# Performance work log

Measured on AMD Instinct MI355X. Metric: run time of the kernel, lower is better.

Reference implementation:

```python
import jax, jax.numpy as jnp
import numpy as np

B, T, F = 1024, 512, 64
P, H = 64, 128  # proj_dim, hidden_size


def _init(key, shape, scale):
    return jax.random.normal(key, shape, dtype=jnp.float32) * scale


def setup_inputs() -> dict:
    key = jax.random.key(0)
    ks = jax.random.split(key, 20)
    sp = 1.0 / np.sqrt(P)
    sh = 1.0 / np.sqrt(H)
    return {
        "x": jax.random.normal(ks[0], (B, T, F), dtype=jnp.float32),
        "lengths": jax.random.randint(ks[1], (B,), 1, T, dtype=jnp.int64),
        # input projection
        "W_proj": _init(ks[2], (P, F), 1.0 / np.sqrt(F)),
        "b_proj": jnp.zeros((P,), jnp.float32),
        # LSTM layer 0 (input P -> hidden H), pytorch gate order i,f,g,o
        "W_ih0": _init(ks[3], (4 * H, P), sh),
        "W_hh0": _init(ks[4], (4 * H, H), sh),
        "b_ih0": _init(ks[5], (4 * H,), sh),
        "b_hh0": _init(ks[6], (4 * H,), sh),
        # LSTM layer 1 (input H -> hidden H)
        "W_ih1": _init(ks[7], (4 * H, H), sh),
        "W_hh1": _init(ks[8], (4 * H, H), sh),
        "b_ih1": _init(ks[9], (4 * H,), sh),
        "b_hh1": _init(ks[10], (4 * H,), sh),
        # MLP head: H -> H//2 -> 1 (dropout is identity in eval)
        "W_h1": _init(ks[11], (H // 2, H), sh),
        "b_h1": jnp.zeros((H // 2,), jnp.float32),
        "W_h2": _init(ks[12], (1, H // 2), 1.0 / np.sqrt(H // 2)),
        "b_h2": jnp.zeros((1,), jnp.float32),
    }


def lstm_layer(x_seq, W_ih, W_hh, b_ih, b_hh):
    # x_seq: [B, T, D]; precompute input contribution for all timesteps
    Hh = W_hh.shape[1]
    xg = jnp.einsum("btd,gd->btg", x_seq, W_ih) + b_ih + b_hh  # [B, T, 4H]
    xg_t = jnp.transpose(xg, (1, 0, 2))  # [T, B, 4H]
    Bn = x_seq.shape[0]
    h0 = jnp.zeros((Bn, Hh), x_seq.dtype)
    c0 = jnp.zeros((Bn, Hh), x_seq.dtype)

    def step(carry, g_in):
        h, c = carry
        g = g_in + h @ W_hh.T
        i, f, gg, o = jnp.split(g, 4, axis=-1)
        i = jax.nn.sigmoid(i)
        f = jax.nn.sigmoid(f)
        gg = jnp.tanh(gg)
        o = jax.nn.sigmoid(o)
        c = f * c + i * gg
        h = o * jnp.tanh(c)
        return (h, c), h

    _, hs = jax.lax.scan(step, (h0, c0), xg_t)  # hs: [T, B, H]
    return jnp.transpose(hs, (1, 0, 2))  # [B, T, H]


def reference(x, lengths, W_proj, b_proj, W_ih0, W_hh0, b_ih0, b_hh0,
              W_ih1, W_hh1, b_ih1, b_hh1, W_h1, b_h1, W_h2, b_h2):
    # eval mode: dropout layers are identity
    proj = jnp.einsum("btf,pf->btp", x, W_proj) + b_proj  # [B, T, P]
    h1 = lstm_layer(proj, W_ih0, W_hh0, b_ih0, b_hh0)
    h2 = lstm_layer(h1, W_ih1, W_hh1, b_ih1, b_hh1)
    last = h2[:, -1, :]  # [B, H]
    hid = jax.nn.relu(last @ W_h1.T + b_h1)
    logits = (hid @ W_h2.T + b_h2).squeeze(-1)  # [B]
    return logits
```

## Files before the change

### kernel.cpp

```cpp
#include <hip/hip_runtime.h>
#include <hip/hip_bf16.h>
#include <stdint.h>

typedef __bf16 bf16x8 __attribute__((ext_vector_type(8)));
typedef float  f32x4  __attribute__((ext_vector_type(4)));

#define BAR()  asm volatile("s_waitcnt lgkmcnt(0)\n\ts_barrier" ::: "memory")

static __device__ __forceinline__ float sigm(float x) {
  return __builtin_amdgcn_rcpf(1.0f + __builtin_amdgcn_exp2f(x * -1.4426950408889634f));
}
static __device__ __forceinline__ float tanh_fast(float x) {
  return 1.0f - 2.0f * __builtin_amdgcn_rcpf(1.0f + __builtin_amdgcn_exp2f(x * 2.8853900817779268f));
}
static __device__ __forceinline__ unsigned short f2bf(float f) {
  return __builtin_bit_cast(unsigned short, (__bf16)f);
}
static __device__ __forceinline__ float bf2f(unsigned short u) {
  union { uint32_t i; float f; } v; v.i = ((uint32_t)u) << 16; return v.f;
}
static __device__ __forceinline__ void async16(const float* g, float* l) {
  __builtin_amdgcn_global_load_lds((__attribute__((address_space(1))) void*)g,
                                   (__attribute__((address_space(3))) void*)l, 16, 0, 0);
}

__global__ __launch_bounds__(512) __attribute__((amdgpu_waves_per_eu(2, 2)))
void fraud_lstm_kernel(
    const float* __restrict__ x,     const float* __restrict__ Wproj,
    const float* __restrict__ bproj, const float* __restrict__ Wih0,
    const float* __restrict__ Whh0,  const float* __restrict__ bih0,
    const float* __restrict__ bhh0,  const float* __restrict__ Wih1,
    const float* __restrict__ Whh1,  const float* __restrict__ bih1,
    const float* __restrict__ bhh1,  const float* __restrict__ Wh1,
    const float* __restrict__ bh1,   const float* __restrict__ Wh2,
    const float* __restrict__ bh2,   float* __restrict__ out)
{
  __shared__ unsigned short sWf[65536];
  __shared__ unsigned short sH0f[2][2048];
  __shared__ unsigned short sH1f[2][2048];
  __shared__ float sXf[3*1024];

  const int tid  = threadIdx.x;
  const int lane = tid & 63;
  const int wid  = tid >> 6;
  const int lr   = lane & 15;
  const int lg   = lane >> 4;
  const int b0   = blockIdx.x * 16;
  const int g0   = wid*16 + lr;

  {
    float* sWp = reinterpret_cast<float*>(sWf);
    for (int i = tid; i < 4096; i += 512) sWp[i] = Wproj[i];
  }
  BAR();

  float w0a[2][4][8];
  #pragma unroll
  for (int kk = 0; kk < 2; ++kk)
    #pragma unroll
    for (int n = 0; n < 4; ++n)
      #pragma unroll
      for (int j = 0; j < 8; ++j) w0a[kk][n][j] = 0.f;
  float bacc[4] = {0.f, 0.f, 0.f, 0.f};
  {
    const float* sWp = reinterpret_cast<const float*>(sWf);
    #pragma unroll 2
    for (int p = 0; p < 64; ++p) {
      float av[4];
      #pragma unroll
      for (int n = 0; n < 4; ++n) av[n] = Wih0[(n*128 + g0)*64 + p];
      float bp = bproj[p];
      #pragma unroll
      for (int n = 0; n < 4; ++n) bacc[n] += av[n] * bp;
      #pragma unroll
      for (int kk = 0; kk < 2; ++kk) {
        f32x4 wa = *(const f32x4*)&sWp[p*64 + kk*32 + lg*8];
        f32x4 wb = *(const f32x4*)&sWp[p*64 + kk*32 + lg*8 + 4];
        #pragma unroll
        for (int n = 0; n < 4; ++n)
          #pragma unroll
          for (int j = 0; j < 4; ++j) {
            w0a[kk][n][j]     += av[n] * wa[j];
            w0a[kk][n][4 + j] += av[n] * wb[j];
          }
      }
    }
  }
  bf16x8 w0f[2][4];
  #pragma unroll
  for (int kk = 0; kk < 2; ++kk)
    #pragma unroll
    for (int n = 0; n < 4; ++n)
      #pragma unroll
      for (int j = 0; j < 8; ++j) w0f[kk][n][j] = (__bf16)w0a[kk][n][j];

  float b0r[4], b1r[4];
  #pragma unroll
  for (int n = 0; n < 4; ++n) {
    const int g = n*128 + g0;
    b0r[n] = bih0[g] + bhh0[g] + bacc[n];
    b1r[n] = bih1[g] + bhh1[g];
  }
  BAR();

  bf16x8 whh0[4][4], wih1[4][4];
  #pragma unroll
  for (int n = 0; n < 4; ++n)
    #pragma unroll
    for (int kk = 0; kk < 4; ++kk) {
      const int ro = (n*128 + g0)*128 + kk*32 + lg*8;
      const float* p0 = Whh0 + ro;
      const float* p1 = Wih1 + ro;
      #pragma unroll
      for (int j = 0; j < 8; ++j) {
        whh0[n][kk][j] = (__bf16)p0[j];
        wih1[n][kk][j] = (__bf16)p1[j];
      }
    }
  #pragma unroll
  for (int n = 0; n < 4; ++n)
    #pragma unroll
    for (int kk = 0; kk < 4; ++kk) {
      const int ro = (n*128 + g0)*128 + kk*32 + lg*8;
      const float* p2 = Whh1 + ro;
      bf16x8 w;
      #pragma unroll
      for (int j = 0; j < 8; ++j) w[j] = (__bf16)p2[j];
      *(bf16x8*)&sWf[((wid*16 + n*4 + kk)*64 + lane)*8] = w;
    }

  for (int i = tid; i < 2048; i += 512) {
    sH0f[0][i] = 0; sH0f[1][i] = 0; sH1f[0][i] = 0; sH1f[1][i] = 0;
  }

  const int schunk = (wid & 3)*64 + lane;
  const int xrow   = schunk >> 4;
  const int xcc    = (schunk & 15) ^ (xrow & 7);
  const float* xg  = x + ((size_t)(b0 + xrow) * 512) * 64 + xcc*4;
  if (wid < 4) {
    async16(xg, &sXf[0*1024 + wid*256]); xg += 64;
    async16(xg, &sXf[1*1024 + wid*256]); xg += 64;
    asm volatile("s_waitcnt vmcnt(1)" ::: "memory");
  }
  BAR();

  const int xo00 = lr*16 + ((lg*2 + 0) ^ (lr & 7));
  const int xo01 = lr*16 + ((lg*2 + 1) ^ (lr & 7));
  const int xo10 = lr*16 + ((8 + lg*2 + 0) ^ (lr & 7));
  const int xo11 = lr*16 + ((8 + lg*2 + 1) ^ (lr & 7));

  const int hbase = (g0 >> 5)*512 + ((g0 >> 3) & 3)*128 + (g0 & 7);

  f32x4 c0r = {0.f,0.f,0.f,0.f}, c1r = {0.f,0.f,0.f,0.f};
  int bufR = 0, bufW = 2;

  #pragma unroll 1
  for (int t = 0; t < 512; ++t) {
    const int cur = t & 1;

    if (wid < 4 && t < 510) { async16(xg, &sXf[bufW*1024 + wid*256]); xg += 64; }

    f32x4 acc0[4];
    #pragma unroll
    for (int n = 0; n < 4; ++n) acc0[n] = f32x4{b0r[n], b0r[n], b0r[n], b0r[n]};

    const f32x4* xb = (const f32x4*)&sXf[bufR*1024];
    #pragma unroll
    for (int kk = 0; kk < 2; ++kk) {
      f32x4 a0 = xb[kk ? xo10 : xo00];
      f32x4 a1 = xb[kk ? xo11 : xo01];
      bf16x8 xa;
      #pragma unroll
      for (int j = 0; j < 4; ++j) { xa[j] = (__bf16)a0[j]; xa[4+j] = (__bf16)a1[j]; }
      #pragma unroll
      for (int n = 0; n < 4; ++n)
        acc0[n] = __builtin_amdgcn_mfma_f32_16x16x32_bf16(xa, w0f[kk][n], acc0[n], 0, 0, 0);
    }
    #pragma unroll
    for (int kk = 0; kk < 4; ++kk) {
      bf16x8 ha = *(const bf16x8*)&sH0f[cur][(kk*64 + lane)*8];
      #pragma unroll
      for (int n = 0; n < 4; ++n)
        acc0[n] = __builtin_amdgcn_mfma_f32_16x16x32_bf16(ha, whh0[n][kk], acc0[n], 0, 0, 0);
    }
    #pragma unroll
    for (int r = 0; r < 4; ++r) {
      float iv = sigm(acc0[0][r]);
      float fv = sigm(acc0[1][r]);
      float gv = tanh_fast(acc0[2][r]);
      float ov = sigm(acc0[3][r]);
      float c  = fv * c0r[r] + iv * gv;
      c0r[r] = c;
      sH0f[cur ^ 1][hbase + (lg*4 + r)*8] = f2bf(ov * tanh_fast(c));
    }
    BAR();

    f32x4 acc1[4];
    #pragma unroll
    for (int n = 0; n < 4; ++n) acc1[n] = f32x4{b1r[n], b1r[n], b1r[n], b1r[n]};
    #pragma unroll
    for (int kk = 0; kk < 4; ++kk) {
      bf16x8 ha = *(const bf16x8*)&sH0f[cur ^ 1][(kk*64 + lane)*8];
      #pragma unroll
      for (int n = 0; n < 4; ++n)
        acc1[n] = __builtin_amdgcn_mfma_f32_16x16x32_bf16(ha, wih1[n][kk], acc1[n], 0, 0, 0);
    }
    #pragma unroll
    for (int kk = 0; kk < 4; ++kk) {
      bf16x8 ha = *(const bf16x8*)&sH1f[cur][(kk*64 + lane)*8];
      #pragma unroll
      for (int n = 0; n < 4; ++n) {
        bf16x8 wf = *(const bf16x8*)&sWf[((wid*16 + n*4 + kk)*64 + lane)*8];
        acc1[n] = __builtin_amdgcn_mfma_f32_16x16x32_bf16(ha, wf, acc1[n], 0, 0, 0);
      }
    }
    #pragma unroll
    for (int r = 0; r < 4; ++r) {
      float iv = sigm(acc1[0][r]);
      float fv = sigm(acc1[1][r]);
      float gv = tanh_fast(acc1[2][r]);
      float ov = sigm(acc1[3][r]);
      float c  = fv * c1r[r] + iv * gv;
      c1r[r] = c;
      sH1f[cur ^ 1][hbase + (lg*4 + r)*8] = f2bf(ov * tanh_fast(c));
    }
    if (wid < 4) {
      if (t < 510) asm volatile("s_waitcnt vmcnt(1)" ::: "memory");
      else         asm volatile("s_waitcnt vmcnt(0)" ::: "memory");
    }
    BAR();

    bufR = (bufR == 2) ? 0 : bufR + 1;
    bufW = (bufW == 2) ? 0 : bufW + 1;
  }

  {
    int row = tid >> 5;
    int j0  = (tid & 31) * 2;
    float a0 = bh1[j0], a1 = bh1[j0 + 1];
    const float* w0 = Wh1 + j0*128;
    const float* w1 = w0 + 128;
    #pragma unroll 8
    for (int k = 0; k < 128; ++k) {
      float hv = bf2f(sH1f[0][(k >> 5)*512 + ((k >> 3) & 3)*128 + row*8 + (k & 7)]);
      a0 += hv * w0[k];
      a1 += hv * w1[k];
    }
    sXf[row*64 + j0]     = fmaxf(a0, 0.f);
    sXf[row*64 + j0 + 1] = fmaxf(a1, 0.f);
  }
  BAR();
  if (tid < 16) {
    float a = bh2[0];
    #pragma unroll 8
    for (int j = 0; j < 64; ++j) a += sXf[tid*64 + j] * Wh2[j];
    out[b0 + tid] = a;
  }
}

extern "C" void kernel_launch(void* const* d_in, const int* in_sizes, int n_in,
                              void* d_out, int out_size, void* d_ws, size_t ws_size,
                              hipStream_t stream) {
  (void)in_sizes; (void)n_in; (void)d_ws; (void)ws_size; (void)out_size;
  const float* x     = (const float*)d_in[0];
  const float* Wproj = (const float*)d_in[2];
  const float* bproj = (const float*)d_in[3];
  const float* Wih0  = (const float*)d_in[4];
  const float* Whh0  = (const float*)d_in[5];
  const float* bih0  = (const float*)d_in[6];
  const float* bhh0  = (const float*)d_in[7];
  const float* Wih1  = (const float*)d_in[8];
  const float* Whh1  = (const float*)d_in[9];
  const float* bih1  = (const float*)d_in[10];
  const float* bhh1  = (const float*)d_in[11];
  const float* Wh1   = (const float*)d_in[12];
  const float* bh1   = (const float*)d_in[13];
  const float* Wh2   = (const float*)d_in[14];
  const float* bh2   = (const float*)d_in[15];
  float* out = (float*)d_out;

  hipLaunchKernelGGL(fraud_lstm_kernel, dim3(64), dim3(512), 0, stream,
                     x, Wproj, bproj, Wih0, Whh0, bih0, bhh0,
                     Wih1, Whh1, bih1, bhh1, Wh1, bh1, Wh2, bh2, out);
}
```

Before: 1.258 ms.

## Skew the two LSTM layers so both compute in one barrier phase per step

Software-pipelines the two stacked LSTM layers so that iteration t computes layer 0 at step t and layer 1 at step t-1 together. A prologue handles layer 0 at step 0 and an epilogue handles the last step of layer 1. This removes one of the two block barriers per timestep and interleaves the independent MFMA chains of both layers, which gives more instruction-level parallelism. The cost is a longer single phase per step, higher register pressure, and more complex buffer indexing, where an error would silently corrupt the result.

New measurement: 1.499 ms. 1.19x slower.

```diff
diff --git a/kernel.cpp b/kernel.cpp
--- a/kernel.cpp
+++ b/kernel.cpp
@@ -152,19 +152,13 @@
   const int hbase = (g0 >> 5)*512 + ((g0 >> 3) & 3)*128 + (g0 & 7);
 
   f32x4 c0r = {0.f,0.f,0.f,0.f}, c1r = {0.f,0.f,0.f,0.f};
-  int bufR = 0, bufW = 2;
-
-  #pragma unroll 1
-  for (int t = 0; t < 512; ++t) {
-    const int cur = t & 1;
-
-    if (wid < 4 && t < 510) { async16(xg, &sXf[bufW*1024 + wid*256]); xg += 64; }
-
+
+  {
+    if (wid < 4) { async16(xg, &sXf[2*1024 + wid*256]); xg += 64; }
     f32x4 acc0[4];
     #pragma unroll
     for (int n = 0; n < 4; ++n) acc0[n] = f32x4{b0r[n], b0r[n], b0r[n], b0r[n]};
-
-    const f32x4* xb = (const f32x4*)&sXf[bufR*1024];
+    const f32x4* xb = (const f32x4*)&sXf[0];
     #pragma unroll
     for (int kk = 0; kk < 2; ++kk) {
       f32x4 a0 = xb[kk ? xo10 : xo00];
@@ -175,13 +169,6 @@
       #pragma unroll
       for (int n = 0; n < 4; ++n)
         acc0[n] = __builtin_amdgcn_mfma_f32_16x16x32_bf16(xa, w0f[kk][n], acc0[n], 0, 0, 0);
-    }
-    #pragma unroll
-    for (int kk = 0; kk < 4; ++kk) {
-      bf16x8 ha = *(const bf16x8*)&sH0f[cur][(kk*64 + lane)*8];
-      #pragma unroll
-      for (int n = 0; n < 4; ++n)
-        acc0[n] = __builtin_amdgcn_mfma_f32_16x16x32_bf16(ha, whh0[n][kk], acc0[n], 0, 0, 0);
     }
     #pragma unroll
     for (int r = 0; r < 4; ++r) {
@@ -191,20 +178,49 @@
       float ov = sigm(acc0[3][r]);
       float c  = fv * c0r[r] + iv * gv;
       c0r[r] = c;
-      sH0f[cur ^ 1][hbase + (lg*4 + r)*8] = f2bf(ov * tanh_fast(c));
-    }
+      sH0f[0][hbase + (lg*4 + r)*8] = f2bf(ov * tanh_fast(c));
+    }
+    if (wid < 4) asm volatile("s_waitcnt vmcnt(1)" ::: "memory");
     BAR();
-
-    f32x4 acc1[4];
-    #pragma unroll
-    for (int n = 0; n < 4; ++n) acc1[n] = f32x4{b1r[n], b1r[n], b1r[n], b1r[n]};
+  }
+  int bufR = 1, bufW = 0;
+
+  #pragma unroll 1
+  for (int t = 1; t < 512; ++t) {
+    const int cur = t & 1;
+
+    if (wid < 4 && t < 510) { async16(xg, &sXf[bufW*1024 + wid*256]); xg += 64; }
+
+    f32x4 acc0[4], acc1[4];
+    #pragma unroll
+    for (int n = 0; n < 4; ++n) {
+      acc0[n] = f32x4{b0r[n], b0r[n], b0r[n], b0r[n]};
+      acc1[n] = f32x4{b1r[n], b1r[n], b1r[n], b1r[n]};
+    }
+
+    const f32x4* xb = (const f32x4*)&sXf[bufR*1024];
+    #pragma unroll
+    for (int kk = 0; kk < 2; ++kk) {
+      f32x4 a0 = xb[kk ? xo10 : xo00];
+      f32x4 a1 = xb[kk ? xo11 : xo01];
+      bf16x8 xa;
+      #pragma unroll
+      for (int j = 0; j < 4; ++j) { xa[j] = (__bf16)a0[j]; xa[4+j] = (__bf16)a1[j]; }
+      #pragma unroll
+      for (int n = 0; n < 4; ++n)
+        acc0[n] = __builtin_amdgcn_mfma_f32_16x16x32_bf16(xa, w0f[kk][n], acc0[n], 0, 0, 0);
+    }
+
     #pragma unroll
     for (int kk = 0; kk < 4; ++kk) {
       bf16x8 ha = *(const bf16x8*)&sH0f[cur ^ 1][(kk*64 + lane)*8];
       #pragma unroll
-      for (int n = 0; n < 4; ++n)
+      for (int n = 0; n < 4; ++n) {
+        acc0[n] = __builtin_amdgcn_mfma_f32_16x16x32_bf16(ha, whh0[n][kk], acc0[n], 0, 0, 0);
         acc1[n] = __builtin_amdgcn_mfma_f32_16x16x32_bf16(ha, wih1[n][kk], acc1[n], 0, 0, 0);
-    }
+      }
+    }
+
     #pragma unroll
     for (int kk = 0; kk < 4; ++kk) {
       bf16x8 ha = *(const bf16x8*)&sH1f[cur][(kk*64 + lane)*8];
@@ -213,6 +229,17 @@
         bf16x8 wf = *(const bf16x8*)&sWf[((wid*16 + n*4 + kk)*64 + lane)*8];
         acc1[n] = __builtin_amdgcn_mfma_f32_16x16x32_bf16(ha, wf, acc1[n], 0, 0, 0);
       }
+    }
+
+    #pragma unroll
+    for (int r = 0; r < 4; ++r) {
+      float iv = sigm(acc0[0][r]);
+      float fv = sigm(acc0[1][r]);
+      float gv = tanh_fast(acc0[2][r]);
+      float ov = sigm(acc0[3][r]);
+      float c  = fv * c0r[r] + iv * gv;
+      c0r[r] = c;
+      sH0f[cur][hbase + (lg*4 + r)*8] = f2bf(ov * tanh_fast(c));
     }
     #pragma unroll
     for (int r = 0; r < 4; ++r) {
@@ -224,6 +251,7 @@
       c1r[r] = c;
       sH1f[cur ^ 1][hbase + (lg*4 + r)*8] = f2bf(ov * tanh_fast(c));
     }
+
     if (wid < 4) {
       if (t < 510) asm volatile("s_waitcnt vmcnt(1)" ::: "memory");
       else         asm volatile("s_waitcnt vmcnt(0)" ::: "memory");
@@ -232,6 +260,39 @@
 
     bufR = (bufR == 2) ? 0 : bufR + 1;
     bufW = (bufW == 2) ? 0 : bufW + 1;
+  }
+
+  {
+    f32x4 acc1[4];
+    #pragma unroll
+    for (int n = 0; n < 4; ++n) acc1[n] = f32x4{b1r[n], b1r[n], b1r[n], b1r[n]};
+    #pragma unroll
+    for (int kk = 0; kk < 4; ++kk) {
+      bf16x8 ha = *(const bf16x8*)&sH0f[1][(kk*64 + lane)*8];
+      #pragma unroll
+      for (int n = 0; n < 4; ++n)
+        acc1[n] = __builtin_amdgcn_mfma_f32_16x16x32_bf16(ha, wih1[n][kk], acc1[n], 0, 0, 0);
+    }
+    #pragma unroll
+    for (int kk = 0; kk < 4; ++kk) {
+      bf16x8 ha = *(const bf16x8*)&sH1f[0][(kk*64 + lane)*8];
+      #pragma unroll
+      for (int n = 0; n < 4; ++n) {
+        bf16x8 wf = *(const bf16x8*)&sWf[((wid*16 + n*4 + kk)*64 + lane)*8];
+        acc1[n] = __builtin_amdgcn_mfma_f32_16x16x32_bf16(ha, wf, acc1[n], 0, 0, 0);
+      }
+    }
+    #pragma unroll
+    for (int r = 0; r < 4; ++r) {
+      float iv = sigm(acc1[0][r]);
+      float fv = sigm(acc1[1][r]);
+      float gv = tanh_fast(acc1[2][r]);
+      float ov = sigm(acc1[3][r]);
+      float c  = fv * c1r[r] + iv * gv;
+      c1r[r] = c;
+      sH1f[1][hbase + (lg*4 + r)*8] = f2bf(ov * tanh_fast(c));
+    }
+    BAR();
   }
 
   {
@@ -242,7 +303,7 @@
     const float* w1 = w0 + 128;
     #pragma unroll 8
     for (int k = 0; k < 128; ++k) {
-      float hv = bf2f(sH1f[0][(k >> 5)*512 + ((k >> 3) & 3)*128 + row*8 + (k & 7)]);
+      float hv = bf2f(sH1f[1][(k >> 5)*512 + ((k >> 3) & 3)*128 + row*8 + (k & 7)]);
       a0 += hv * w0[k];
       a1 += hv * w1[k];
     }
```

## Skew LSTM layers by one step to drop a barrier per timestep

Applied to the files above, without the earlier changes.

Layer 1 now runs one timestep behind layer 0, so each loop iteration computes layer-0 step t and layer-1 step t-1 from h buffers written in the previous iteration, needing only one barrier per step instead of two. An epilogue finishes the last layer-1 step. The x staging layout is rewritten so the async loads land already in MFMA operand order, removing the swizzled index math, and sched_barriers pin instruction ordering. The risk is subtle buffer-parity errors in the skewed schedule, and the sched_barriers may limit the compiler's interleaving.

After: 1.126 ms. 10.5% less time.

```diff
diff --git a/kernel.cpp b/kernel.cpp
--- a/kernel.cpp
+++ b/kernel.cpp
@@ -6,6 +6,7 @@
 typedef float  f32x4  __attribute__((ext_vector_type(4)));
 
 #define BAR()  asm volatile("s_waitcnt lgkmcnt(0)\n\ts_barrier" ::: "memory")
+#define SB()   __builtin_amdgcn_sched_barrier(0)
 
 static __device__ __forceinline__ float sigm(float x) {
   return __builtin_amdgcn_rcpf(1.0f + __builtin_amdgcn_exp2f(x * -1.4426950408889634f));
@@ -38,7 +39,7 @@
   __shared__ unsigned short sWf[65536];
   __shared__ unsigned short sH0f[2][2048];
   __shared__ unsigned short sH1f[2][2048];
-  __shared__ float sXf[3*1024];
+  __shared__ float sXB[3*1024];
 
   const int tid  = threadIdx.x;
   const int lane = tid & 63;
@@ -133,23 +134,17 @@
     sH0f[0][i] = 0; sH0f[1][i] = 0; sH1f[0][i] = 0; sH1f[1][i] = 0;
   }
 
-  const int schunk = (wid & 3)*64 + lane;
-  const int xrow   = schunk >> 4;
-  const int xcc    = (schunk & 15) ^ (xrow & 7);
-  const float* xg  = x + ((size_t)(b0 + xrow) * 512) * 64 + xcc*4;
+  const float* xw = x + (size_t)(b0 + (lane & 15)) * (512*64)
+                      + ((wid >> 1) & 1) * 32 + (lane >> 4) * 8 + (wid & 1) * 4;
   if (wid < 4) {
-    async16(xg, &sXf[0*1024 + wid*256]); xg += 64;
-    async16(xg, &sXf[1*1024 + wid*256]); xg += 64;
+    async16(xw,      &sXB[0*1024 + wid*256]);
+    async16(xw + 64, &sXB[1*1024 + wid*256]);
     asm volatile("s_waitcnt vmcnt(1)" ::: "memory");
   }
   BAR();
 
-  const int xo00 = lr*16 + ((lg*2 + 0) ^ (lr & 7));
-  const int xo01 = lr*16 + ((lg*2 + 1) ^ (lr & 7));
-  const int xo10 = lr*16 + ((8 + lg*2 + 0) ^ (lr & 7));
-  const int xo11 = lr*16 + ((8 + lg*2 + 1) ^ (lr & 7));
-
-  const int hbase = (g0 >> 5)*512 + ((g0 >> 3) & 3)*128 + (g0 & 7);
+  const int hwb = (g0 >> 5)*1024 + ((g0 >> 3) & 3)*256 + (g0 & 7)*2 + lg*64;
+  const int lb  = lane * 16;
 
   f32x4 c0r = {0.f,0.f,0.f,0.f}, c1r = {0.f,0.f,0.f,0.f};
   int bufR = 0, bufW = 2;
@@ -158,62 +153,118 @@
   for (int t = 0; t < 512; ++t) {
     const int cur = t & 1;
 
-    if (wid < 4 && t < 510) { async16(xg, &sXf[bufW*1024 + wid*256]); xg += 64; }
+    if (wid < 4 && t < 510) async16(xw + (t + 2)*64, &sXB[bufW*1024 + wid*256]);
 
     f32x4 acc0[4];
     #pragma unroll
     for (int n = 0; n < 4; ++n) acc0[n] = f32x4{b0r[n], b0r[n], b0r[n], b0r[n]};
-
-    const f32x4* xb = (const f32x4*)&sXf[bufR*1024];
+    const char* xp = (const char*)sXB + bufR*4096 + lb;
     #pragma unroll
     for (int kk = 0; kk < 2; ++kk) {
-      f32x4 a0 = xb[kk ? xo10 : xo00];
-      f32x4 a1 = xb[kk ? xo11 : xo01];
+      f32x4 a0 = *(const f32x4*)(xp + kk*2048);
+      f32x4 a1 = *(const f32x4*)(xp + kk*2048 + 1024);
       bf16x8 xa;
       #pragma unroll
       for (int j = 0; j < 4; ++j) { xa[j] = (__bf16)a0[j]; xa[4+j] = (__bf16)a1[j]; }
       #pragma unroll
       for (int n = 0; n < 4; ++n)
         acc0[n] = __builtin_amdgcn_mfma_f32_16x16x32_bf16(xa, w0f[kk][n], acc0[n], 0, 0, 0);
-    }
-    #pragma unroll
-    for (int kk = 0; kk < 4; ++kk) {
-      bf16x8 ha = *(const bf16x8*)&sH0f[cur][(kk*64 + lane)*8];
+      SB();
+    }
+    const char* h0p = (const char*)sH0f[cur ^ 1] + lb;
+    #pragma unroll
+    for (int kk = 0; kk < 4; ++kk) {
+      bf16x8 ha = *(const bf16x8*)(h0p + kk*1024);
       #pragma unroll
       for (int n = 0; n < 4; ++n)
         acc0[n] = __builtin_amdgcn_mfma_f32_16x16x32_bf16(ha, whh0[n][kk], acc0[n], 0, 0, 0);
-    }
-    #pragma unroll
-    for (int r = 0; r < 4; ++r) {
-      float iv = sigm(acc0[0][r]);
-      float fv = sigm(acc0[1][r]);
-      float gv = tanh_fast(acc0[2][r]);
-      float ov = sigm(acc0[3][r]);
-      float c  = fv * c0r[r] + iv * gv;
-      c0r[r] = c;
-      sH0f[cur ^ 1][hbase + (lg*4 + r)*8] = f2bf(ov * tanh_fast(c));
-    }
-    BAR();
-
+      SB();
+    }
+    {
+      char* hw = (char*)sH0f[cur] + hwb;
+      #pragma unroll
+      for (int r = 0; r < 4; ++r) {
+        float iv = sigm(acc0[0][r]);
+        float fv = sigm(acc0[1][r]);
+        float gv = tanh_fast(acc0[2][r]);
+        float ov = sigm(acc0[3][r]);
+        float c  = fv * c0r[r] + iv * gv;
+        c0r[r] = c;
+        *(unsigned short*)(hw + r*16) = f2bf(ov * tanh_fast(c));
+      }
+    }
+    SB();
     f32x4 acc1[4];
     #pragma unroll
     for (int n = 0; n < 4; ++n) acc1[n] = f32x4{b1r[n], b1r[n], b1r[n], b1r[n]};
     #pragma unroll
     for (int kk = 0; kk < 4; ++kk) {
-      bf16x8 ha = *(const bf16x8*)&sH0f[cur ^ 1][(kk*64 + lane)*8];
+      bf16x8 ha = *(const bf16x8*)(h0p + kk*1024);
       #pragma unroll
       for (int n = 0; n < 4; ++n)
         acc1[n] = __builtin_amdgcn_mfma_f32_16x16x32_bf16(ha, wih1[n][kk], acc1[n], 0, 0, 0);
-    }
-    #pragma unroll
-    for (int kk = 0; kk < 4; ++kk) {
-      bf16x8 ha = *(const bf16x8*)&sH1f[cur][(kk*64 + lane)*8];
+      SB();
+    }
+    const char* h1p = (const char*)sH1f[cur] + lb;
+    const char* wp  = (const char*)sWf + wid*16384 + lb;
+    #pragma unroll
+    for (int kk = 0; kk < 4; ++kk) {
+      bf16x8 ha = *(const bf16x8*)(h1p + kk*1024);
       #pragma unroll
       for (int n = 0; n < 4; ++n) {
-        bf16x8 wf = *(const bf16x8*)&sWf[((wid*16 + n*4 + kk)*64 + lane)*8];
+        bf16x8 wf = *(const bf16x8*)(wp + (n*4 + kk)*1024);
         acc1[n] = __builtin_amdgcn_mfma_f32_16x16x32_bf16(ha, wf, acc1[n], 0, 0, 0);
       }
-    }
+      SB();
+    }
+    if (t > 0) {
+      char* hw = (char*)sH1f[cur ^ 1] + hwb;
+      #pragma unroll
+      for (int r = 0; r < 4; ++r) {
+        float iv = sigm(acc1[0][r]);
+        float fv = sigm(acc1[1][r]);
+        float gv = tanh_fast(acc1[2][r]);
+        float ov = sigm(acc1[3][r]);
+        float c  = fv * c1r[r] + iv * gv;
+        c1r[r] = c;
+        *(unsigned short*)(hw + r*16) = f2bf(ov * tanh_fast(c));
+      }
+    }
+
+    if (wid < 4) {
+      if (t < 510) asm volatile("s_waitcnt vmcnt(1)" ::: "memory");
+      else         asm volatile("s_waitcnt vmcnt(0)" ::: "memory");
+    }
+    BAR();
+
+    bufR = (bufR == 2) ? 0 : bufR + 1;
+    bufW = (bufW == 2) ? 0 : bufW + 1;
+  }
+
+  {
+    f32x4 acc1[4];
+    #pragma unroll
+    for (int n = 0; n < 4; ++n) acc1[n] = f32x4{b1r[n], b1r[n], b1r[n], b1r[n]};
+    const char* h0p = (const char*)sH0f[1] + lb;
+    #pragma unroll
+    for (int kk = 0; kk < 4; ++kk) {
+      bf16x8 ha = *(const bf16x8*)(h0p + kk*1024);
+      #pragma unroll
+      for (int n = 0; n < 4; ++n)
+        acc1[n] = __builtin_amdgcn_mfma_f32_16x16x32_bf16(ha, wih1[n][kk], acc1[n], 0, 0, 0);
+    }
+    const char* h1p = (const char*)sH1f[0] + lb;
+    const char* wp  = (const char*)sWf + wid*16384 + lb;
+    #pragma unroll
+    for (int kk = 0; kk < 4; ++kk) {
+      bf16x8 ha = *(const bf16x8*)(h1p + kk*1024);
+      #pragma unroll
+      for (int n = 0; n < 4; ++n) {
+        bf16x8 wf = *(const bf16x8*)(wp + (n*4 + kk)*1024);
+        acc1[n] = __builtin_amdgcn_mfma_f32_16x16x32_bf16(ha, wf, acc1[n], 0, 0, 0);
+      }
+    }
+    char* hw = (char*)sH1f[1] + hwb;
     #pragma unroll
     for (int r = 0; r < 4; ++r) {
       float iv = sigm(acc1[0][r]);
@@ -222,16 +273,9 @@
       float ov = sigm(acc1[3][r]);
       float c  = fv * c1r[r] + iv * gv;
       c1r[r] = c;
-      sH1f[cur ^ 1][hbase + (lg*4 + r)*8] = f2bf(ov * tanh_fast(c));
-    }
-    if (wid < 4) {
-      if (t < 510) asm volatile("s_waitcnt vmcnt(1)" ::: "memory");
-      else         asm volatile("s_waitcnt vmcnt(0)" ::: "memory");
+      *(unsigned short*)(hw + r*16) = f2bf(ov * tanh_fast(c));
     }
     BAR();
-
-    bufR = (bufR == 2) ? 0 : bufR + 1;
-    bufW = (bufW == 2) ? 0 : bufW + 1;
   }
 
   {
@@ -242,18 +286,18 @@
     const float* w1 = w0 + 128;
     #pragma unroll 8
     for (int k = 0; k < 128; ++k) {
-      float hv = bf2f(sH1f[0][(k >> 5)*512 + ((k >> 3) & 3)*128 + row*8 + (k & 7)]);
+      float hv = bf2f(sH1f[1][(k >> 5)*512 + ((k >> 3) & 3)*128 + row*8 + (k & 7)]);
       a0 += hv * w0[k];
       a1 += hv * w1[k];
     }
-    sXf[row*64 + j0]     = fmaxf(a0, 0.f);
-    sXf[row*64 + j0 + 1] = fmaxf(a1, 0.f);
+    sXB[row*64 + j0]     = fmaxf(a0, 0.f);
+    sXB[row*64 + j0 + 1] = fmaxf(a1, 0.f);
   }
   BAR();
   if (tid < 16) {
     float a = bh2[0];
     #pragma unroll 8
-    for (int j = 0; j < 64; ++j) a += sXf[tid*64 + j] * Wh2[j];
+    for (int j = 0; j < 64; ++j) a += sXB[tid*64 + j] * Wh2[j];
     out[b0 + tid] = a;
   }
 }
```

## Split LSTM layers into producer/consumer blocks linked by a global ring buffer

Applied to the files above, without the earlier changes.

The kernel now launches 128 blocks: the first 64 run layer 0 and stream each step's h0 into a ring buffer in global workspace, and the other 64 run layer 1, consuming those slots through acquire/release flags. The two layers then run as a cross-block pipeline instead of in series inside one block, which halves the per-step critical path and keeps Whh1 in registers rather than LDS. In exchange it adds a global round trip and spin-waits on every step, and correctness depends on all 128 blocks being co-resident and on the workspace being large enough. Sched barriers are also inserted to pin the MFMA ordering.

After: 1.497 ms. 19.0% more time.

```diff
diff --git a/kernel.cpp b/kernel.cpp
--- a/kernel.cpp
+++ b/kernel.cpp
@@ -6,6 +6,7 @@
 typedef float  f32x4  __attribute__((ext_vector_type(4)));
 
 #define BAR()  asm volatile("s_waitcnt lgkmcnt(0)\n\ts_barrier" ::: "memory")
+#define SB()   __builtin_amdgcn_sched_barrier(0)
 
 static __device__ __forceinline__ float sigm(float x) {
   return __builtin_amdgcn_rcpf(1.0f + __builtin_amdgcn_exp2f(x * -1.4426950408889634f));
@@ -23,9 +24,15 @@
   __builtin_amdgcn_global_load_lds((__attribute__((address_space(1))) void*)g,
                                    (__attribute__((address_space(3))) void*)l, 16, 0, 0);
 }
+static __device__ __forceinline__ uint32_t aload_acq(uint32_t* p) {
+  return __hip_atomic_load(p, __ATOMIC_ACQUIRE, __HIP_MEMORY_SCOPE_AGENT);
+}
+static __device__ __forceinline__ void astore_rel(uint32_t* p, uint32_t v) {
+  __hip_atomic_store(p, v, __ATOMIC_RELEASE, __HIP_MEMORY_SCOPE_AGENT);
+}
 
 __global__ __launch_bounds__(512) __attribute__((amdgpu_waves_per_eu(2, 2)))
-void fraud_lstm_kernel(
+void fraud_lstm_split(
     const float* __restrict__ x,     const float* __restrict__ Wproj,
     const float* __restrict__ bproj, const float* __restrict__ Wih0,
     const float* __restrict__ Whh0,  const float* __restrict__ bih0,
@@ -33,49 +40,55 @@
     const float* __restrict__ Whh1,  const float* __restrict__ bih1,
     const float* __restrict__ bhh1,  const float* __restrict__ Wh1,
     const float* __restrict__ bh1,   const float* __restrict__ Wh2,
-    const float* __restrict__ bh2,   float* __restrict__ out)
+    const float* __restrict__ bh2,   float* __restrict__ out,
+    uint32_t* __restrict__ wsp, int D)
 {
-  __shared__ unsigned short sWf[65536];
+  __shared__ float sStage[4096];
   __shared__ unsigned short sH0f[2][2048];
   __shared__ unsigned short sH1f[2][2048];
-  __shared__ float sXf[3*1024];
+  __shared__ float sXB[2][1024];
+  __shared__ uint32_t sFlag;
 
   const int tid  = threadIdx.x;
   const int lane = tid & 63;
   const int wid  = tid >> 6;
   const int lr   = lane & 15;
   const int lg   = lane >> 4;
-  const int b0   = blockIdx.x * 16;
   const int g0   = wid*16 + lr;
-
-  {
-    float* sWp = reinterpret_cast<float*>(sWf);
-    for (int i = tid; i < 4096; i += 512) sWp[i] = Wproj[i];
-  }
-  BAR();
-
-  float w0a[2][4][8];
-  #pragma unroll
-  for (int kk = 0; kk < 2; ++kk)
-    #pragma unroll
-    for (int n = 0; n < 4; ++n)
-      #pragma unroll
-      for (int j = 0; j < 8; ++j) w0a[kk][n][j] = 0.f;
-  float bacc[4] = {0.f, 0.f, 0.f, 0.f};
-  {
-    const float* sWp = reinterpret_cast<const float*>(sWf);
+  const int hwb  = (g0 >> 5)*1024 + ((g0 >> 3) & 3)*256 + (g0 & 7)*2 + lg*64;
+  const int lb   = lane * 16;
+  const int Dm   = D - 1;
+
+  if (blockIdx.x < 64) {
+    const int p  = blockIdx.x;
+    const int b0 = p * 16;
+    uint32_t* prodf = wsp + p*16;
+    uint32_t* consf = wsp + 1024 + p*16;
+    char* slots = (char*)wsp + 8192 + (size_t)p * D * 4096;
+
+    for (int i = tid; i < 4096; i += 512) sStage[i] = Wproj[i];
+    __syncthreads();
+
+    float w0a[2][4][8];
+    #pragma unroll
+    for (int kk = 0; kk < 2; ++kk)
+      #pragma unroll
+      for (int n = 0; n < 4; ++n)
+        #pragma unroll
+        for (int j = 0; j < 8; ++j) w0a[kk][n][j] = 0.f;
+    float bacc[4] = {0.f, 0.f, 0.f, 0.f};
     #pragma unroll 2
-    for (int p = 0; p < 64; ++p) {
+    for (int pp = 0; pp < 64; ++pp) {
       float av[4];
       #pragma unroll
-      for (int n = 0; n < 4; ++n) av[n] = Wih0[(n*128 + g0)*64 + p];
-      float bp = bproj[p];
+      for (int n = 0; n < 4; ++n) av[n] = Wih0[(n*128 + g0)*64 + pp];
+      float bp = bproj[pp];
       #pragma unroll
       for (int n = 0; n < 4; ++n) bacc[n] += av[n] * bp;
       #pragma unroll
       for (int kk = 0; kk < 2; ++kk) {
-        f32x4 wa = *(const f32x4*)&sWp[p*64 + kk*32 + lg*8];
-        f32x4 wb = *(const f32x4*)&sWp[p*64 + kk*32 + lg*8 + 4];
+        f32x4 wa = *(const f32x4*)&sStage[pp*64 + kk*32 + lg*8];
+        f32x4 wb = *(const f32x4*)&sStage[pp*64 + kk*32 + lg*8 + 4];
         #pragma unroll
         for (int n = 0; n < 4; ++n)
           #pragma unroll
@@ -85,183 +98,231 @@
           }
       }
     }
+    bf16x8 w0f[2][4];
+    #pragma unroll
+    for (int kk = 0; kk < 2; ++kk)
+      #pragma unroll
+      for (int n = 0; n < 4; ++n)
+        #pragma unroll
+        for (int j = 0; j < 8; ++j) w0f[kk][n][j] = (__bf16)w0a[kk][n][j];
+    float b0r[4];
+    #pragma unroll
+    for (int n = 0; n < 4; ++n) {
+      const int g = n*128 + g0;
+      b0r[n] = bih0[g] + bhh0[g] + bacc[n];
+    }
+
+    bf16x8 whh0[4][4];
+    #pragma unroll
+    for (int n = 0; n < 4; ++n)
+      #pragma unroll
+      for (int kk = 0; kk < 4; ++kk) {
+        const float* p0 = Whh0 + (n*128 + g0)*128 + kk*32 + lg*8;
+        #pragma unroll
+        for (int j = 0; j < 8; ++j) whh0[n][kk][j] = (__bf16)p0[j];
+      }
+
+    for (int i = tid; i < 2048; i += 512) { sH0f[0][i] = 0; sH0f[1][i] = 0; }
+
+    const float* xw = x + (size_t)(b0 + (lane & 15)) * (512*64)
+                        + ((wid >> 1) & 1) * 32 + (lane >> 4) * 8 + (wid & 1) * 4;
+    if (wid < 4) async16(xw, &sXB[0][wid*256]);
+    __syncthreads();
+
+    f32x4 c0r = {0.f,0.f,0.f,0.f};
+    uint32_t kc = 0;
+
+    #pragma unroll 1
+    for (int t = 0; t < 512; ++t) {
+      const int cur = t & 1;
+      if (wid < 4 && t < 511) async16(xw + (t + 1)*64, &sXB[cur ^ 1][wid*256]);
+
+      const char* xp  = (const char*)sXB[cur] + lb;
+      const char* h0p = (const char*)sH0f[cur ^ 1] + lb;
+      char* hw0 = (char*)sH0f[cur] + hwb;
+
+      f32x4 acc0[4];
+      #pragma unroll
+      for (int n = 0; n < 4; ++n) acc0[n] = f32x4{b0r[n], b0r[n], b0r[n], b0r[n]};
+      #pragma unroll
+      for (int kk = 0; kk < 2; ++kk) {
+        f32x4 a0 = *(const f32x4*)(xp + kk*2048);
+        f32x4 a1 = *(const f32x4*)(xp + kk*2048 + 1024);
+        bf16x8 xa;
+        #pragma unroll
+        for (int j = 0; j < 4; ++j) { xa[j] = (__bf16)a0[j]; xa[4+j] = (__bf16)a1[j]; }
+        #pragma unroll
+        for (int n = 0; n < 4; ++n)
+          acc0[n] = __builtin_amdgcn_mfma_f32_16x16x32_bf16(xa, w0f[kk][n], acc0[n], 0, 0, 0);
+        SB();
+      }
+      #pragma unroll
+      for (int kk = 0; kk < 4; ++kk) {
+        bf16x8 ha = *(const bf16x8*)(h0p + kk*1024);
+        #pragma unroll
+        for (int n = 0; n < 4; ++n)
+          acc0[n] = __builtin_amdgcn_mfma_f32_16x16x32_bf16(ha, whh0[n][kk], acc0[n], 0, 0, 0);
+        SB();
+      }
+      #pragma unroll
+      for (int r = 0; r < 4; ++r) {
+        float iv = sigm(acc0[0][r]);
+        float fv = sigm(acc0[1][r]);
+        float gv = tanh_fast(acc0[2][r]);
+        float ov = sigm(acc0[3][r]);
+        float c  = fv * c0r[r] + iv * gv;
+        c0r[r] = c;
+        *(unsigned short*)(hw0 + r*16) = f2bf(ov * tanh_fast(c));
+      }
+      SB();
+
+      if (t >= D && (int)kc < t + 1 - D) {
+        if (tid == 0) {
+          uint32_t v = aload_acq(consf);
+          while ((int)v < t + 1 - D) { __builtin_amdgcn_s_sleep(2); v = aload_acq(consf); }
+          sFlag = v;
+        }
+        __syncthreads();
+        kc = sFlag;
+      }
+      __syncthreads();
+      *(uint64_t*)(slots + (size_t)(t & Dm)*4096 + tid*8) =
+          *(const uint64_t*)((const char*)sH0f[cur] + tid*8);
+      __syncthreads();
+      if (tid == 0) astore_rel(prodf, (uint32_t)(t + 1));
+    }
+    return;
   }
-  bf16x8 w0f[2][4];
-  #pragma unroll
-  for (int kk = 0; kk < 2; ++kk)
+
+  {
+    const int p  = blockIdx.x - 64;
+    const int b0 = p * 16;
+    uint32_t* prodf = wsp + p*16;
+    uint32_t* consf = wsp + 1024 + p*16;
+    const char* slots = (const char*)wsp + 8192 + (size_t)p * D * 4096;
+
+    bf16x8 wih1[4][4], whh1[4][4];
     #pragma unroll
     for (int n = 0; n < 4; ++n)
       #pragma unroll
-      for (int j = 0; j < 8; ++j) w0f[kk][n][j] = (__bf16)w0a[kk][n][j];
-
-  float b0r[4], b1r[4];
-  #pragma unroll
-  for (int n = 0; n < 4; ++n) {
-    const int g = n*128 + g0;
-    b0r[n] = bih0[g] + bhh0[g] + bacc[n];
-    b1r[n] = bih1[g] + bhh1[g];
-  }
-  BAR();
-
-  bf16x8 whh0[4][4], wih1[4][4];
-  #pragma unroll
-  for (int n = 0; n < 4; ++n)
-    #pragma unroll
-    for (int kk = 0; kk < 4; ++kk) {
-      const int ro = (n*128 + g0)*128 + kk*32 + lg*8;
-      const float* p0 = Whh0 + ro;
-      const float* p1 = Wih1 + ro;
-      #pragma unroll
-      for (int j = 0; j < 8; ++j) {
-        whh0[n][kk][j] = (__bf16)p0[j];
-        wih1[n][kk][j] = (__bf16)p1[j];
-      }
-    }
-  #pragma unroll
-  for (int n = 0; n < 4; ++n)
-    #pragma unroll
-    for (int kk = 0; kk < 4; ++kk) {
-      const int ro = (n*128 + g0)*128 + kk*32 + lg*8;
-      const float* p2 = Whh1 + ro;
-      bf16x8 w;
-      #pragma unroll
-      for (int j = 0; j < 8; ++j) w[j] = (__bf16)p2[j];
-      *(bf16x8*)&sWf[((wid*16 + n*4 + kk)*64 + lane)*8] = w;
-    }
-
-  for (int i = tid; i < 2048; i += 512) {
-    sH0f[0][i] = 0; sH0f[1][i] = 0; sH1f[0][i] = 0; sH1f[1][i] = 0;
-  }
-
-  const int schunk = (wid & 3)*64 + lane;
-  const int xrow   = schunk >> 4;
-  const int xcc    = (schunk & 15) ^ (xrow & 7);
-  const float* xg  = x + ((size_t)(b0 + xrow) * 512) * 64 + xcc*4;
-  if (wid < 4) {
-    async16(xg, &sXf[0*1024 + wid*256]); xg += 64;
-    async16(xg, &sXf[1*1024 + wid*256]); xg += 64;
-    asm volatile("s_waitcnt vmcnt(1)" ::: "memory");
-  }
-  BAR();
-
-  const int xo00 = lr*16 + ((lg*2 + 0) ^ (lr & 7));
-  const int xo01 = lr*16 + ((lg*2 + 1) ^ (lr & 7));
-  const int xo10 = lr*16 + ((8 + lg*2 + 0) ^ (lr & 7));
-  const int xo11 = lr*16 + ((8 + lg*2 + 1) ^ (lr & 7));
-
-  const int hbase = (g0 >> 5)*512 + ((g0 >> 3) & 3)*128 + (g0 & 7);
-
-  f32x4 c0r = {0.f,0.f,0.f,0.f}, c1r = {0.f,0.f,0.f,0.f};
-  int bufR = 0, bufW = 2;
-
-  #pragma unroll 1
-  for (int t = 0; t < 512; ++t) {
-    const int cur = t & 1;
-
-    if (wid < 4 && t < 510) { async16(xg, &sXf[bufW*1024 + wid*256]); xg += 64; }
-
-    f32x4 acc0[4];
-    #pragma unroll
-    for (int n = 0; n < 4; ++n) acc0[n] = f32x4{b0r[n], b0r[n], b0r[n], b0r[n]};
-
-    const f32x4* xb = (const f32x4*)&sXf[bufR*1024];
-    #pragma unroll
-    for (int kk = 0; kk < 2; ++kk) {
-      f32x4 a0 = xb[kk ? xo10 : xo00];
-      f32x4 a1 = xb[kk ? xo11 : xo01];
-      bf16x8 xa;
-      #pragma unroll
-      for (int j = 0; j < 4; ++j) { xa[j] = (__bf16)a0[j]; xa[4+j] = (__bf16)a1[j]; }
-      #pragma unroll
-      for (int n = 0; n < 4; ++n)
-        acc0[n] = __builtin_amdgcn_mfma_f32_16x16x32_bf16(xa, w0f[kk][n], acc0[n], 0, 0, 0);
-    }
-    #pragma unroll
-    for (int kk = 0; kk < 4; ++kk) {
-      bf16x8 ha = *(const bf16x8*)&sH0f[cur][(kk*64 + lane)*8];
-      #pragma unroll
-      for (int n = 0; n < 4; ++n)
-        acc0[n] = __builtin_amdgcn_mfma_f32_16x16x32_bf16(ha, whh0[n][kk], acc0[n], 0, 0, 0);
-    }
-    #pragma unroll
-    for (int r = 0; r < 4; ++r) {
-      float iv = sigm(acc0[0][r]);
-      float fv = sigm(acc0[1][r]);
-      float gv = tanh_fast(acc0[2][r]);
-      float ov = sigm(acc0[3][r]);
-      float c  = fv * c0r[r] + iv * gv;
-      c0r[r] = c;
-      sH0f[cur ^ 1][hbase + (lg*4 + r)*8] = f2bf(ov * tanh_fast(c));
+      for (int kk = 0; kk < 4; ++kk) {
+        const int ro = (n*128 + g0)*128 + kk*32 + lg*8;
+        const float* p1 = Wih1 + ro;
+        const float* p2 = Whh1 + ro;
+        #pragma unroll
+        for (int j = 0; j < 8; ++j) {
+          wih1[n][kk][j] = (__bf16)p1[j];
+          whh1[n][kk][j] = (__bf16)p2[j];
+        }
+      }
+    float b1r[4];
+    #pragma unroll
+    for (int n = 0; n < 4; ++n) {
+      const int g = n*128 + g0;
+      b1r[n] = bih1[g] + bhh1[g];
+    }
+    for (int i = tid; i < 2048; i += 512) { sH1f[0][i] = 0; sH1f[1][i] = 0; }
+    __syncthreads();
+
+    f32x4 c1r = {0.f,0.f,0.f,0.f};
+    uint32_t kp = 0;
+
+    #pragma unroll 1
+    for (int t = 0; t < 512; ++t) {
+      const int cur = t & 1;
+
+      if (kp < (uint32_t)(t + 1)) {
+        if (tid == 0) {
+          uint32_t v = aload_acq(prodf);
+          while (v < (uint32_t)(t + 1)) { __builtin_amdgcn_s_sleep(2); v = aload_acq(prodf); }
+          sFlag = v;
+        }
+        __syncthreads();
+        kp = sFlag;
+      }
+
+      const char* sl = slots + (size_t)(t & Dm)*4096 + lb;
+      bf16x8 h0a0 = *(const bf16x8*)(sl);
+      bf16x8 h0a1 = *(const bf16x8*)(sl + 1024);
+      bf16x8 h0a2 = *(const bf16x8*)(sl + 2048);
+      bf16x8 h0a3 = *(const bf16x8*)(sl + 3072);
+      SB();
+
+      f32x4 acc1[4];
+      #pragma unroll
+      for (int n = 0; n < 4; ++n) acc1[n] = f32x4{b1r[n], b1r[n], b1r[n], b1r[n]};
+
+      const char* h1p = (const char*)sH1f[cur ^ 1] + lb;
+      #pragma unroll
+      for (int kk = 0; kk < 4; ++kk) {
+        bf16x8 ha = *(const bf16x8*)(h1p + kk*1024);
+        #pragma unroll
+        for (int n = 0; n < 4; ++n)
+          acc1[n] = __builtin_amdgcn_mfma_f32_16x16x32_bf16(ha, whh1[n][kk], acc1[n], 0, 0, 0);
+        SB();
+      }
+      #pragma unroll
+      for (int n = 0; n < 4; ++n)
+        acc1[n] = __builtin_amdgcn_mfma_f32_16x16x32_bf16(h0a0, wih1[n][0], acc1[n], 0, 0, 0);
+      SB();
+      #pragma unroll
+      for (int n = 0; n < 4; ++n)
+        acc1[n] = __builtin_amdgcn_mfma_f32_16x16x32_bf16(h0a1, wih1[n][1], acc1[n], 0, 0, 0);
+      SB();
+      #pragma unroll
+      for (int n = 0; n < 4; ++n)
+        acc1[n] = __builtin_amdgcn_mfma_f32_16x16x32_bf16(h0a2, wih1[n][2], acc1[n], 0, 0, 0);
+      SB();
+      #pragma unroll
+      for (int n = 0; n < 4; ++n)
+        acc1[n] = __builtin_amdgcn_mfma_f32_16x16x32_bf16(h0a3, wih1[n][3], acc1[n], 0, 0, 0);
+      SB();
+
+      char* hw = (char*)sH1f[cur] + hwb;
+      #pragma unroll
+      for (int r = 0; r < 4; ++r) {
+        float iv = sigm(acc1[0][r]);
+        float fv = sigm(acc1[1][r]);
+        float gv = tanh_fast(acc1[2][r]);
+        float ov = sigm(acc1[3][r]);
+        float c  = fv * c1r[r] + iv * gv;
+        c1r[r] = c;
+        *(unsigned short*)(hw + r*16) = f2bf(ov * tanh_fast(c));
+      }
+
+      __syncthreads();
+      if (tid == 0) astore_rel(consf, (uint32_t)(t + 1));
+    }
+
+    {
+      int row = tid >> 5;
+      int j0  = (tid & 31) * 2;
+      float a0 = bh1[j0], a1 = bh1[j0 + 1];
+      const float* w0 = Wh1 + j0*128;
+      const float* w1 = w0 + 128;
+      #pragma unroll 8
+      for (int k = 0; k < 128; ++k) {
+        float hv = bf2f(sH1f[1][(k >> 5)*512 + ((k >> 3) & 3)*128 + row*8 + (k & 7)]);
+        a0 += hv * w0[k];
+        a1 += hv * w1[k];
+      }
+      sStage[row*64 + j0]     = fmaxf(a0, 0.f);
+      sStage[row*64 + j0 + 1] = fmaxf(a1, 0.f);
     }
     BAR();
-
-    f32x4 acc1[4];
-    #pragma unroll
-    for (int n = 0; n < 4; ++n) acc1[n] = f32x4{b1r[n], b1r[n], b1r[n], b1r[n]};
-    #pragma unroll
-    for (int kk = 0; kk < 4; ++kk) {
-      bf16x8 ha = *(const bf16x8*)&sH0f[cur ^ 1][(kk*64 + lane)*8];
-      #pragma unroll
-      for (int n = 0; n < 4; ++n)
-        acc1[n] = __builtin_amdgcn_mfma_f32_16x16x32_bf16(ha, wih1[n][kk], acc1[n], 0, 0, 0);
-    }
-    #pragma unroll
-    for (int kk = 0; kk < 4; ++kk) {
-      bf16x8 ha = *(const bf16x8*)&sH1f[cur][(kk*64 + lane)*8];
-      #pragma unroll
-      for (int n = 0; n < 4; ++n) {
-        bf16x8 wf = *(const bf16x8*)&sWf[((wid*16 + n*4 + kk)*64 + lane)*8];
-        acc1[n] = __builtin_amdgcn_mfma_f32_16x16x32_bf16(ha, wf, acc1[n], 0, 0, 0);
-      }
-    }
-    #pragma unroll
-    for (int r = 0; r < 4; ++r) {
-      float iv = sigm(acc1[0][r]);
-      float fv = sigm(acc1[1][r]);
-      float gv = tanh_fast(acc1[2][r]);
-      float ov = sigm(acc1[3][r]);
-      float c  = fv * c1r[r] + iv * gv;
-      c1r[r] = c;
-      sH1f[cur ^ 1][hbase + (lg*4 + r)*8] = f2bf(ov * tanh_fast(c));
-    }
-    if (wid < 4) {
-      if (t < 510) asm volatile("s_waitcnt vmcnt(1)" ::: "memory");
-      else         asm volatile("s_waitcnt vmcnt(0)" ::: "memory");
-    }
-    BAR();
-
-    bufR = (bufR == 2) ? 0 : bufR + 1;
-    bufW = (bufW == 2) ? 0 : bufW + 1;
-  }
-
-  {
-    int row = tid >> 5;
-    int j0  = (tid & 31) * 2;
-    float a0 = bh1[j0], a1 = bh1[j0 + 1];
-    const float* w0 = Wh1 + j0*128;
-    const float* w1 = w0 + 128;
-    #pragma unroll 8
-    for (int k = 0; k < 128; ++k) {
-      float hv = bf2f(sH1f[0][(k >> 5)*512 + ((k >> 3) & 3)*128 + row*8 + (k & 7)]);
-      a0 += hv * w0[k];
-      a1 += hv * w1[k];
-    }
-    sXf[row*64 + j0]     = fmaxf(a0, 0.f);
-    sXf[row*64 + j0 + 1] = fmaxf(a1, 0.f);
-  }
-  BAR();
-  if (tid < 16) {
-    float a = bh2[0];
-    #pragma unroll 8
-    for (int j = 0; j < 64; ++j) a += sXf[tid*64 + j] * Wh2[j];
-    out[b0 + tid] = a;
+    if (tid < 16) {
+      float a = bh2[0];
+      #pragma unroll 8
+      for (int j = 0; j < 64; ++j) a += sStage[tid*64 + j] * Wh2[j];
+      out[b0 + tid] = a;
+    }
   }
 }
 
 extern "C" void kernel_launch(void* const* d_in, const int* in_sizes, int n_in,
                               void* d_out, int out_size, void* d_ws, size_t ws_size,
                               hipStream_t stream) {
-  (void)in_sizes; (void)n_in; (void)d_ws; (void)ws_size; (void)out_size;
+  (void)in_sizes; (void)n_in; (void)out_size;
   const float* x     = (const float*)d_in[0];
   const float* Wproj = (const float*)d_in[2];
   const float* bproj = (const float*)d_in[3];
@@ -278,8 +339,15 @@
   const float* Wh2   = (const float*)d_in[14];
   const float* bh2   = (const float*)d_in[15];
   float* out = (float*)d_out;
-
-  hipLaunchKernelGGL(fraud_lstm_kernel, dim3(64), dim3(512), 0, stream,
+  uint32_t* wsp = (uint32_t*)d_ws;
+
+  int D = (ws_size >= 8192 + (size_t)64*8*4096) ? 8
+        : (ws_size >= 8192 + (size_t)64*4*4096) ? 4
+        : (ws_size >= 8192 + (size_t)64*2*4096) ? 2 : 1;
+
+  hipMemsetAsync(d_ws, 0, 8192, stream);
+
+  hipLaunchKernelGGL(fraud_lstm_split, dim3(128), dim3(512), 0, stream,
                      x, Wproj, bproj, Wih0, Whh0, bih0, bhh0,
-                     Wih1, Whh1, bih1, bhh1, Wh1, bh1, Wh2, bh2, out);
-}
+                     Wih1, Whh1, bih1, bhh1, Wh1, bh1, Wh2, bh2, out, wsp, D);
+}
```
